# Kernel tuning notes

Measured on AMD Instinct MI355X. Metric: run time of the kernel, lower is better.

## Reference

```python
import jax, jax.numpy as jnp
import numpy as np

B, L, H, E, K, P, V = 32, 64, 1024, 8, 2, 8, 12000
OUT = 2 * P  # moe_gauss out_features
COEF = 0.1   # moe_loss_coef


def setup_inputs() -> dict:
    key = jax.random.key(0)
    ks = jax.random.split(key, 6)
    s = 0.02
    return {
        "query_repr": jax.random.normal(ks[0], (B, H), jnp.float32),
        "h": jax.random.normal(ks[1], (B, L, H), jnp.float32),
        "gate_w1": jax.random.normal(ks[2], (H, H // 2), jnp.float32) * s,
        "gate_b1": jnp.zeros((H // 2,), jnp.float32),
        "gate_w2": jax.random.normal(ks[3], (H // 2, E), jnp.float32) * s,
        "gate_b2": jnp.zeros((E,), jnp.float32),
        "gauss_w": jax.random.normal(ks[4], (E, OUT, H), jnp.float32) * s,
        "gauss_b": jnp.zeros((E, OUT), jnp.float32),
        "comp_w": jax.random.normal(ks[5], (E, V, H), jnp.float32) * s,
        "comp_b": jnp.zeros((E, V), jnp.float32),
    }


def reference(query_repr, h, gate_w1, gate_b1, gate_w2, gate_b2,
              gauss_w, gauss_b, comp_w, comp_b):
    # --- QueryGuidedGating: MLP -> top-k -> softmax -> scatter ---
    hid = jax.nn.relu(query_repr @ gate_w1 + gate_b1)          # [B, H/2]
    logits = hid @ gate_w2 + gate_b2                            # [B, E]
    top_vals, top_idx = jax.lax.top_k(logits, K)                # [B, K]
    top_gates = jax.nn.softmax(top_vals, axis=-1)               # [B, K]
    rows = jnp.arange(logits.shape[0])[:, None]
    gates = jnp.zeros_like(logits).at[rows, top_idx].set(top_gates)  # [B, E]

    # --- balance_loss: cv = std(importance)/(mean+eps) * coef (torch std is ddof=1) ---
    importance = gates.sum(0)                                   # [E]
    moe_loss = (jnp.std(importance, ddof=1) / (importance.mean() + 1e-10)) * COEF

    # --- QueryGuidedMoELinear: per-sample mixed weight, then bmm ---
    mixed_w = jnp.einsum('be,eoi->boi', gates, gauss_w)         # [B, OUT, H]
    mixed_b = jnp.einsum('be,eo->bo', gates, gauss_b)           # [B, OUT]
    h_last = h[:, -1]                                           # [B, H]
    gauss_param = jax.nn.sigmoid(jnp.einsum('bi,boi->bo', h_last, mixed_w) + mixed_b)

    # --- _moe_comp_forward: gated accumulation over experts (avoids [B,E,L,V]) ---
    comp = jnp.zeros((h.shape[0], h.shape[1], comp_w.shape[1]), h.dtype)
    for e in range(E):  # fixed small expert count
        expert_out = jnp.einsum('blh,vh->blv', h, comp_w[e]) + comp_b[e]
        comp = comp + gates[:, e, None, None] * expert_out

    return gauss_param, comp, moe_loss
```

## Files before the change

kernel.cpp:

```cpp
#include <hip/hip_runtime.h>
#include <hip/hip_bf16.h>
#include <cmath>

#define B_   32
#define L_   64
#define H_   1024
#define E_   8
#define V_   12000
#define OUT_ 16
#define HID_ 512

#define BN  96
#define BK  64
#define LDK 72
#define NVT (V_ / BN)

#define COMP_OFF 512
#define LOSS_OFF (512 + B_ * L_ * V_)

using f32x4  = __attribute__((ext_vector_type(4))) float;
using bf16x8 = __attribute__((ext_vector_type(8))) short;
using s16x4  = __attribute__((ext_vector_type(4))) short;

__device__ __forceinline__ short f2bf(float f) {
  unsigned u = __builtin_bit_cast(unsigned, f);
  u = (u + 0x7FFFu + ((u >> 16) & 1u)) >> 16;
  return (short)u;
}

typedef __attribute__((address_space(1))) void gvoid_t;
typedef __attribute__((address_space(3))) void lvoid_t;
#define GLOAD16(g, l) __builtin_amdgcn_global_load_lds((gvoid_t*)(g), (lvoid_t*)(l), 16, 0, 0)

__global__ __launch_bounds__(256) void k_conv(const float* __restrict__ src,
                                              short* __restrict__ dst, int n8) {
  size_t i = (size_t)blockIdx.x * 256 + threadIdx.x;
  const size_t stride = (size_t)gridDim.x * 256;
  for (; i < (size_t)n8; i += stride) {
    const f32x4 a = ((const f32x4*)src)[2 * i];
    const f32x4 b = ((const f32x4*)src)[2 * i + 1];
    bf16x8 o;
    o[0] = f2bf(a[0]); o[1] = f2bf(a[1]); o[2] = f2bf(a[2]); o[3] = f2bf(a[3]);
    o[4] = f2bf(b[0]); o[5] = f2bf(b[1]); o[6] = f2bf(b[2]); o[7] = f2bf(b[3]);
    ((bf16x8*)dst)[i] = o;
  }
}

__global__ __launch_bounds__(256) void k_gate(
    const float* __restrict__ q,  const float* __restrict__ w1,
    const float* __restrict__ b1, const float* __restrict__ w2,
    const float* __restrict__ b2, const float* __restrict__ h,
    const float* __restrict__ gw, const float* __restrict__ gb,
    float* __restrict__ gates,    float* __restrict__ egate,
    int* __restrict__ eidx,       float* __restrict__ out) {
  __shared__ __align__(16) float qs[H_];
  __shared__ __align__(16) float hid[HID_];
  __shared__ __align__(16) float red[256][8];
  __shared__ float sg[2];
  __shared__ int   se[2];
  const int t = threadIdx.x;
  const int b = blockIdx.x;

  ((f32x4*)qs)[t] = ((const f32x4*)(q + (size_t)b * H_))[t];
  __syncthreads();

  {
    const int jq = t & 127, ih = t >> 7;
    f32x4 acc = {0.f, 0.f, 0.f, 0.f};
    const float* wp = w1 + (size_t)(ih * 512) * HID_ + 4 * jq;
    for (int i = 0; i < 512; ++i) {
      acc += qs[ih * 512 + i] * *(const f32x4*)(wp + (size_t)i * HID_);
    }
    *(f32x4*)&red[t][0] = acc;
  }
  __syncthreads();
  if (t < 128) {
    f32x4 a = *(f32x4*)&red[t][0];
    a += *(f32x4*)&red[t + 128][0];
    a += *(const f32x4*)(b1 + 4 * t);
    f32x4 r;
    #pragma unroll
    for (int c = 0; c < 4; ++c) r[c] = fmaxf(a[c], 0.f);
    *(f32x4*)&hid[4 * t] = r;
  }
  __syncthreads();

  {
    const float h0 = hid[t], h1 = hid[t + 256];
    const float* w2a = w2 + (size_t)t * E_;
    const float* w2b = w2 + (size_t)(t + 256) * E_;
    #pragma unroll
    for (int e = 0; e < 8; ++e) red[t][e] = h0 * w2a[e] + h1 * w2b[e];
  }
  __syncthreads();
  for (int s = 128; s > 0; s >>= 1) {
    if (t < s) {
      #pragma unroll
      for (int e = 0; e < 8; ++e) red[t][e] += red[t + s][e];
    }
    __syncthreads();
  }

  if (t == 0) {
    float lg[8];
    #pragma unroll
    for (int e = 0; e < 8; ++e) lg[e] = red[0][e] + b2[e];
    int e1 = 0;
    #pragma unroll
    for (int e = 1; e < 8; ++e) if (lg[e] > lg[e1]) e1 = e;
    int e2 = (e1 == 0) ? 1 : 0;
    #pragma unroll
    for (int e = 0; e < 8; ++e) if (e != e1 && lg[e] > lg[e2]) e2 = e;
    const float x2 = expf(lg[e2] - lg[e1]);
    const float g1 = 1.f / (1.f + x2);
    const float g2 = x2 / (1.f + x2);
    #pragma unroll
    for (int e = 0; e < 8; ++e)
      gates[b * E_ + e] = (e == e1) ? g1 : (e == e2) ? g2 : 0.f;
    egate[2 * b] = g1; egate[2 * b + 1] = g2;
    eidx[2 * b]  = e1; eidx[2 * b + 1]  = e2;
    sg[0] = g1; sg[1] = g2; se[0] = e1; se[1] = e2;
  }
  __syncthreads();

  {
    const float gg1 = sg[0], gg2 = sg[1];
    const int ee1 = se[0], ee2 = se[1];
    const int o = t >> 4, sub = t & 15;
    const float* hl = h  + ((size_t)(b * L_ + (L_ - 1))) * H_ + sub * 64;
    const float* wa = gw + ((size_t)(ee1 * OUT_ + o)) * H_ + sub * 64;
    const float* wb = gw + ((size_t)(ee2 * OUT_ + o)) * H_ + sub * 64;
    float p = 0.f;
    #pragma unroll 4
    for (int i = 0; i < 64; i += 4) {
      const f32x4 hv = *(const f32x4*)(hl + i);
      const f32x4 va = *(const f32x4*)(wa + i);
      const f32x4 vb = *(const f32x4*)(wb + i);
      const f32x4 w  = gg1 * va + gg2 * vb;
      p += hv[0] * w[0] + hv[1] * w[1] + hv[2] * w[2] + hv[3] * w[3];
    }
    float* red1 = &red[0][0];
    red1[t] = p;
    __syncthreads();
    if (t < 16) {
      float s = gg1 * gb[ee1 * OUT_ + t] + gg2 * gb[ee2 * OUT_ + t];
      #pragma unroll
      for (int k2 = 0; k2 < 16; ++k2) s += red1[t * 16 + k2];
      out[b * OUT_ + t] = 1.f / (1.f + expf(-s));
    }
  }
}

__global__ __launch_bounds__(64) void k_loss(const float* __restrict__ gates,
                                             float* __restrict__ out) {
  __shared__ float imp[8];
  const int t = threadIdx.x;
  if (t < 8) {
    float s = 0.f;
    for (int b = 0; b < B_; ++b) s += gates[b * E_ + t];
    imp[t] = s;
  }
  __syncthreads();
  if (t == 0) {
    float m = 0.f;
    #pragma unroll
    for (int e = 0; e < 8; ++e) m += imp[e];
    m *= 0.125f;
    float var = 0.f;
    #pragma unroll
    for (int e = 0; e < 8; ++e) { const float d = imp[e] - m; var += d * d; }
    var *= (1.f / 7.f);
    out[LOSS_OFF] = sqrtf(var) / (m + 1e-10f) * 0.1f;
  }
}

__global__ __launch_bounds__(256) void k_comp_fast(
    const short* __restrict__ hbf, const float* __restrict__ cw,
    const float* __restrict__ cb,  const float* __restrict__ egate,
    const int* __restrict__ eidx,  float* __restrict__ out) {
  __shared__ __align__(16) short As[2][64 * 64];
  __shared__ __align__(16) short Bs[96 * 64];
  const int t  = threadIdx.x;
  const int id  = blockIdx.x;
  const int xcd = id & 7;
  const int pos = id >> 3;
  const int b   = pos & 31;
  const int g   = pos >> 5;
  const int vt  = g * 8 + xcd;
  if (vt >= NVT) return;
  const int e1 = eidx[2 * b], e2 = eidx[2 * b + 1];
  const float g1 = egate[2 * b], g2 = egate[2 * b + 1];

  const int srow = t >> 3, schunk = t & 7;
  const unsigned soff = (unsigned)((schunk << 4) ^ ((srow & 7) << 4));
  const char* sAk = (const char*)hbf + ((size_t)b * 64 + srow) * 2048 + soff;
  char* dA0 = (char*)&As[0][0] + t * 16;
  char* dA1 = (char*)&As[1][0] + t * 16;

  const float* wB1 = cw + ((size_t)e1 * V_ + (size_t)vt * BN + srow) * H_ + schunk * 8;
  const float* wB2 = cw + ((size_t)e2 * V_ + (size_t)vt * BN + srow) * H_ + schunk * 8;
  short* dBp = Bs + srow * 64 + ((schunk ^ (srow & 7)) << 3);

  f32x4 r1[3][2], r2[3][2];

#define LOADB(koff)                                                          \
  do {                                                                       \
    _Pragma("unroll")                                                        \
    for (int p = 0; p < 3; ++p) {                                            \
      r1[p][0] = *(const f32x4*)(wB1 + (size_t)p * 32 * H_ + (koff));        \
      r1[p][1] = *(const f32x4*)(wB1 + (size_t)p * 32 * H_ + (koff) + 4);    \
      r2[p][0] = *(const f32x4*)(wB2 + (size_t)p * 32 * H_ + (koff));        \
      r2[p][1] = *(const f32x4*)(wB2 + (size_t)p * 32 * H_ + (koff) + 4);    \
    }                                                                        \
  } while (0)

#define WRITEB()                                                             \
  do {                                                                       \
    _Pragma("unroll")                                                        \
    for (int p = 0; p < 3; ++p) {                                            \
      const f32x4 m0 = g1 * r1[p][0] + g2 * r2[p][0];                        \
      const f32x4 m1 = g1 * r1[p][1] + g2 * r2[p][1];                        \
      bf16x8 o;                                                              \
      o[0] = f2bf(m0[0]); o[1] = f2bf(m0[1]);                                \
      o[2] = f2bf(m0[2]); o[3] = f2bf(m0[3]);                                \
      o[4] = f2bf(m1[0]); o[5] = f2bf(m1[1]);                                \
      o[6] = f2bf(m1[2]); o[7] = f2bf(m1[3]);                                \
      *(bf16x8*)(dBp + p * 32 * 64) = o;                                     \
    }                                                                        \
  } while (0)

  const int lane = t & 63, wv = t >> 6;
  const int lr = lane & 15, quad = lane >> 4;
  const int mh = wv & 1, ng = wv >> 1;
  int offA[2][2], offB[3][2];
  #pragma unroll
  for (int mf = 0; mf < 2; ++mf) {
    const int ra = mh * 32 + mf * 16 + lr;
    offA[mf][0] = ra * 64 + (((quad    ) ^ (ra & 7)) << 3);
    offA[mf][1] = ra * 64 + (((quad ^ 4) ^ (ra & 7)) << 3);
  }
  #pragma unroll
  for (int nn = 0; nn < 3; ++nn) {
    const int rb = (ng * 3 + nn) * 16 + lr;
    offB[nn][0] = rb * 64 + (((quad    ) ^ (rb & 7)) << 3);
    offB[nn][1] = rb * 64 + (((quad ^ 4) ^ (rb & 7)) << 3);
  }

  f32x4 acc[2][3];
  #pragma unroll
  for (int i = 0; i < 2; ++i)
    #pragma unroll
    for (int j = 0; j < 3; ++j) acc[i][j] = (f32x4){0.f, 0.f, 0.f, 0.f};

  GLOAD16(sAk,         dA0);
  GLOAD16(sAk + 65536, dA0 + 4096);
  sAk += 128;
  LOADB(0);
  int koff = 64;

  for (int t16 = 0; t16 < 16; ++t16) {
    WRITEB();
    __syncthreads();

    if (t16 < 15) {
      char* dAn = (t16 & 1) ? dA0 : dA1;
      GLOAD16(sAk,         dAn);
      GLOAD16(sAk + 65536, dAn + 4096);
      sAk += 128;
      LOADB(koff);
      koff += 64;
    }
    const short* Asb = &As[t16 & 1][0];
    #pragma unroll
    for (int ks = 0; ks < 2; ++ks) {
      const bf16x8 a0 = *(const bf16x8*)(Asb + offA[0][ks]);
      const bf16x8 a1 = *(const bf16x8*)(Asb + offA[1][ks]);
      #pragma unroll
      for (int nn = 0; nn < 3; ++nn) {
        const bf16x8 wbm = *(const bf16x8*)(Bs + offB[nn][ks]);
        acc[0][nn] = __builtin_amdgcn_mfma_f32_16x16x32_bf16(a0, wbm, acc[0][nn], 0, 0, 0);
        acc[1][nn] = __builtin_amdgcn_mfma_f32_16x16x32_bf16(a1, wbm, acc[1][nn], 0, 0, 0);
      }
    }
    __syncthreads();
  }

  #pragma unroll
  for (int nn = 0; nn < 3; ++nn) {
    const int v = vt * BN + (ng * 3 + nn) * 16 + lr;
    const float bias = g1 * cb[e1 * V_ + v] + g2 * cb[e2 * V_ + v];
    #pragma unroll
    for (int mf = 0; mf < 2; ++mf) {
      const int lbase = mh * 32 + mf * 16 + quad * 4;
      float* op = out + COMP_OFF + ((size_t)(b * L_ + lbase)) * V_ + v;
      #pragma unroll
      for (int rr = 0; rr < 4; ++rr)
        op[(size_t)rr * V_] = acc[mf][nn][rr] + bias;
    }
  }
#undef LOADB
#undef WRITEB
}

__global__ __launch_bounds__(256) void k_comp(
    const float* __restrict__ h,     const float* __restrict__ cw,
    const float* __restrict__ cbp,   const float* __restrict__ egate,
    const int* __restrict__ eidx,    float* __restrict__ out) {
  __shared__ __align__(16) short As[L_ * LDK];
  __shared__ __align__(16) short Bs[BN * LDK];
  const int t  = threadIdx.x;
  const int b  = blockIdx.x;
  const int vt = blockIdx.y;
  const int e1 = eidx[2 * b], e2 = eidx[2 * b + 1];
  const float g1 = egate[2 * b], g2 = egate[2 * b + 1];

  const float* hrow = h + ((size_t)b * L_ + (t >> 2)) * H_ + ((t & 3) * 16);
  const float* w1p  = cw + ((size_t)e1 * V_ + (size_t)vt * BN) * H_;
  const float* w2p  = cw + ((size_t)e2 * V_ + (size_t)vt * BN) * H_;

  f32x4 acc[6];
  #pragma unroll
  for (int i = 0; i < 6; ++i) acc[i] = (f32x4){0.f, 0.f, 0.f, 0.f};

  const int wv = t >> 6;
  const int lane = t & 63;
  const int lr = lane & 15, quad = lane >> 4;
  const short* Ap = As + (wv * 16 + lr) * LDK;
  const short* Bp = Bs + lr * LDK;

  const int wr = t >> 3;
  const int wc = (t & 7) * 8;

  for (int k0 = 0; k0 < H_; k0 += BK) {
    {
      const float* src = hrow + k0;
      short* dst = As + (t >> 2) * LDK + (t & 3) * 16;
      #pragma unroll
      for (int c = 0; c < 16; c += 4) {
        const f32x4 v = *(const f32x4*)(src + c);
        s16x4 sv;
        sv[0] = f2bf(v[0]); sv[1] = f2bf(v[1]);
        sv[2] = f2bf(v[2]); sv[3] = f2bf(v[3]);
        *(s16x4*)(dst + c) = sv;
      }
    }
    #pragma unroll
    for (int p = 0; p < 3; ++p) {
      const int r = p * 32 + wr;
      const float* s1 = w1p + (size_t)r * H_ + k0 + wc;
      const float* s2 = w2p + (size_t)r * H_ + k0 + wc;
      short* dst = Bs + r * LDK + wc;
      #pragma unroll
      for (int c = 0; c < 8; c += 4) {
        const f32x4 a  = *(const f32x4*)(s1 + c);
        const f32x4 bb = *(const f32x4*)(s2 + c);
        const f32x4 m  = g1 * a + g2 * bb;
        s16x4 sv;
        sv[0] = f2bf(m[0]); sv[1] = f2bf(m[1]);
        sv[2] = f2bf(m[2]); sv[3] = f2bf(m[3]);
        *(s16x4*)(dst + c) = sv;
      }
    }
    __syncthreads();

    #pragma unroll
    for (int ks = 0; ks < BK; ks += 32) {
      const bf16x8 af = *(const bf16x8*)(Ap + ks + quad * 8);
      #pragma unroll
      for (int n = 0; n < 6; ++n) {
        const bf16x8 bf = *(const bf16x8*)(Bp + n * 16 * LDK + ks + quad * 8);
        acc[n] = __builtin_amdgcn_mfma_f32_16x16x32_bf16(af, bf, acc[n], 0, 0, 0);
      }
    }
    __syncthreads();
  }

  #pragma unroll
  for (int n = 0; n < 6; ++n) {
    const int v = vt * BN + n * 16 + lr;
    const float bias = g1 * cbp[e1 * V_ + v] + g2 * cbp[e2 * V_ + v];
    #pragma unroll
    for (int r = 0; r < 4; ++r) {
      const int l = wv * 16 + quad * 4 + r;
      out[COMP_OFF + ((size_t)(b * L_ + l)) * V_ + v] = acc[n][r] + bias;
    }
  }
}

extern "C" void kernel_launch(void* const* d_in, const int* in_sizes, int n_in,
                              void* d_out, int out_size, void* d_ws, size_t ws_size,
                              hipStream_t stream) {
  const float* q   = (const float*)d_in[0];
  const float* h   = (const float*)d_in[1];
  const float* w1  = (const float*)d_in[2];
  const float* b1  = (const float*)d_in[3];
  const float* w2  = (const float*)d_in[4];
  const float* b2  = (const float*)d_in[5];
  const float* gw  = (const float*)d_in[6];
  const float* gb  = (const float*)d_in[7];
  const float* cw  = (const float*)d_in[8];
  const float* cbp = (const float*)d_in[9];
  float* out = (float*)d_out;

  float* F     = (float*)d_ws;
  float* gates = F;
  float* egate = F + 256;
  int*   eidx  = (int*)(F + 320);

  const size_t HBF_OFF = 4096;
  const size_t HBF_BYTES = (size_t)B_ * L_ * H_ * 2;
  const size_t WS_NEED = HBF_OFF + HBF_BYTES;

  k_gate<<<B_, 256, 0, stream>>>(q, w1, b1, w2, b2, h, gw, gb, gates, egate, eidx, out);
  k_loss<<<1, 64, 0, stream>>>(gates, out);

  if (ws_size >= WS_NEED) {
    short* hbf = (short*)((char*)d_ws + HBF_OFF);
    k_conv<<<256, 256, 0, stream>>>(h, hbf, (int)((size_t)B_ * L_ * H_ / 8));
    k_comp_fast<<<4096, 256, 0, stream>>>(hbf, cw, cbp, egate, eidx, out);
  } else {
    k_comp<<<dim3(B_, V_ / BN), 256, 0, stream>>>(h, cw, cbp, egate, eidx, out);
  }
}
```

Measured before the change: 767.9 us.

## Deepen weight prefetch to two stages with manual waitcnt and barriers

Expert weights are now prefetched two K-steps ahead into a double-buffered register set instead of one step ahead. The main loop is fully unrolled, and __syncthreads is replaced by raw s_barrier plus explicit vmcnt/lgkmcnt waits so outstanding global loads can stay in flight across the barrier. The aim is to hide the latency of the fp32 weight stream behind the MFMA work. In exchange, register pressure roughly doubles for the prefetch buffers, and the correctness of the hand-written waitcnt values depends on the compiler's load ordering.

```diff
diff --git a/kernel.cpp b/kernel.cpp
--- a/kernel.cpp
+++ b/kernel.cpp
@@ -194,32 +194,30 @@
   const int srow = t >> 3, schunk = t & 7;
   const unsigned soff = (unsigned)((schunk << 4) ^ ((srow & 7) << 4));
   const char* sAk = (const char*)hbf + ((size_t)b * 64 + srow) * 2048 + soff;
-  char* dA0 = (char*)&As[0][0] + t * 16;
-  char* dA1 = (char*)&As[1][0] + t * 16;
 
   const float* wB1 = cw + ((size_t)e1 * V_ + (size_t)vt * BN + srow) * H_ + schunk * 8;
   const float* wB2 = cw + ((size_t)e2 * V_ + (size_t)vt * BN + srow) * H_ + schunk * 8;
   short* dBp = Bs + srow * 64 + ((schunk ^ (srow & 7)) << 3);
 
-  f32x4 r1[3][2], r2[3][2];
-
-#define LOADB(koff)                                                          \
+  f32x4 pa[2][3][2], pb[2][3][2];
+
+#define LOADB(S, koff)                                                       \
   do {                                                                       \
     _Pragma("unroll")                                                        \
     for (int p = 0; p < 3; ++p) {                                            \
-      r1[p][0] = *(const f32x4*)(wB1 + (size_t)p * 32 * H_ + (koff));        \
-      r1[p][1] = *(const f32x4*)(wB1 + (size_t)p * 32 * H_ + (koff) + 4);    \
-      r2[p][0] = *(const f32x4*)(wB2 + (size_t)p * 32 * H_ + (koff));        \
-      r2[p][1] = *(const f32x4*)(wB2 + (size_t)p * 32 * H_ + (koff) + 4);    \
+      pa[S][p][0] = *(const f32x4*)(wB1 + (size_t)p * 32 * H_ + (koff));     \
+      pa[S][p][1] = *(const f32x4*)(wB1 + (size_t)p * 32 * H_ + (koff) + 4); \
+      pb[S][p][0] = *(const f32x4*)(wB2 + (size_t)p * 32 * H_ + (koff));     \
+      pb[S][p][1] = *(const f32x4*)(wB2 + (size_t)p * 32 * H_ + (koff) + 4); \
     }                                                                        \
   } while (0)
 
-#define WRITEB()                                                             \
+#define WRITEB(S)                                                            \
   do {                                                                       \
     _Pragma("unroll")                                                        \
     for (int p = 0; p < 3; ++p) {                                            \
-      const f32x4 m0 = g1 * r1[p][0] + g2 * r2[p][0];                        \
-      const f32x4 m1 = g1 * r1[p][1] + g2 * r2[p][1];                        \
+      const f32x4 m0 = g1 * pa[S][p][0] + g2 * pb[S][p][0];                  \
+      const f32x4 m1 = g1 * pa[S][p][1] + g2 * pb[S][p][1];                  \
       bf16x8 o;                                                              \
       o[0] = f2bf(m0[0]); o[1] = f2bf(m0[1]);                                \
       o[2] = f2bf(m0[2]); o[3] = f2bf(m0[3]);                                \
@@ -252,37 +250,56 @@
     #pragma unroll
     for (int j = 0; j < 3; ++j) acc[i][j] = (f32x4){0.f, 0.f, 0.f, 0.f};
 
-  GLOAD16(sAk,         dA0);
-  GLOAD16(sAk + 65536, dA0 + 4096);
-  sAk += 128;
-  LOADB(0);
-  int koff = 64;
-
-  for (int t16 = 0; t16 < 16; ++t16) {
-    WRITEB();
-    __syncthreads();
-
-    if (t16 < 15) {
-      char* dAn = (t16 & 1) ? dA0 : dA1;
+  {
+    char* dA0 = (char*)&As[0][0] + t * 16;
+    GLOAD16(sAk,         dA0);
+    GLOAD16(sAk + 65536, dA0 + 4096);
+    sAk += 128;
+  }
+  asm volatile("" ::: "memory");
+  LOADB(0, 0);
+  asm volatile("" ::: "memory");
+  LOADB(1, 64);
+  asm volatile("" ::: "memory");
+
+  #pragma unroll
+  for (int u = 0; u < 16; ++u) {
+    WRITEB(u & 1);
+    asm volatile("s_waitcnt lgkmcnt(0)" ::: "memory");
+    __builtin_amdgcn_s_barrier();
+
+    if (u == 0)       { asm volatile("" ::: "memory"); }
+    else if (u < 15)  { asm volatile("s_waitcnt vmcnt(12)" ::: "memory"); }
+    else              { asm volatile("s_waitcnt vmcnt(0)"  ::: "memory"); }
+
+    if (u < 15) {
+      char* dAn = (char*)&As[(u + 1) & 1][0] + t * 16;
       GLOAD16(sAk,         dAn);
       GLOAD16(sAk + 65536, dAn + 4096);
       sAk += 128;
-      LOADB(koff);
-      koff += 64;
-    }
-    const short* Asb = &As[t16 & 1][0];
-    #pragma unroll
-    for (int ks = 0; ks < 2; ++ks) {
-      const bf16x8 a0 = *(const bf16x8*)(Asb + offA[0][ks]);
-      const bf16x8 a1 = *(const bf16x8*)(Asb + offA[1][ks]);
-      #pragma unroll
-      for (int nn = 0; nn < 3; ++nn) {
-        const bf16x8 wbm = *(const bf16x8*)(Bs + offB[nn][ks]);
-        acc[0][nn] = __builtin_amdgcn_mfma_f32_16x16x32_bf16(a0, wbm, acc[0][nn], 0, 0, 0);
-        acc[1][nn] = __builtin_amdgcn_mfma_f32_16x16x32_bf16(a1, wbm, acc[1][nn], 0, 0, 0);
+      asm volatile("" ::: "memory");
+    }
+    if (u < 14) {
+      LOADB((u & 1), (u + 2) * 64);
+    }
+    asm volatile("" ::: "memory");
+
+    {
+      const short* Asb = &As[u & 1][0];
+      #pragma unroll
+      for (int ks = 0; ks < 2; ++ks) {
+        const bf16x8 a0 = *(const bf16x8*)(Asb + offA[0][ks]);
+        const bf16x8 a1 = *(const bf16x8*)(Asb + offA[1][ks]);
+        #pragma unroll
+        for (int nn = 0; nn < 3; ++nn) {
+          const bf16x8 wbm = *(const bf16x8*)(Bs + offB[nn][ks]);
+          acc[0][nn] = __builtin_amdgcn_mfma_f32_16x16x32_bf16(a0, wbm, acc[0][nn], 0, 0, 0);
+          acc[1][nn] = __builtin_amdgcn_mfma_f32_16x16x32_bf16(a1, wbm, acc[1][nn], 0, 0, 0);
+        }
       }
     }
-    __syncthreads();
+    asm volatile("" ::: "memory");
+    __builtin_amdgcn_s_barrier();
   }
 
   #pragma unroll
```

Result: slower. 819.1 us (+6.7%).
